# Kernel optimization log

Hardware: AMD Instinct MI355X
Metric: run time of the kernel (lower is better)

The kernel has to match this reference:

```python
import jax, jax.numpy as jnp
import numpy as np

HID, NH, QLR, KVLR, QK, VH, RH = 7168, 128, 1536, 512, 128, 128, 64
EPS = 1.1920929e-07  # torch.finfo(float32).eps, RMSNorm eps=None default
ROPE_BASE = 10000.0


def _rmsnorm(x, w):
    return x * jax.lax.rsqrt(jnp.mean(x * x, axis=-1, keepdims=True) + EPS) * w


def _rope_tables(seq_len, dim):
    inv_freq = 1.0 / (ROPE_BASE ** (np.arange(0, dim, 2, dtype=np.float32) / dim))
    t = np.arange(seq_len, dtype=np.float32)
    freqs = np.outer(t, inv_freq)          # [S, dim/2]
    emb = np.concatenate([freqs, freqs], -1)  # [S, dim]
    return jnp.asarray(np.cos(emb)), jnp.asarray(np.sin(emb))


def _apply_rope(x, cos, sin):
    # x: [B, H, S, D]; rotate-half convention matching the torch module
    d = x.shape[-1]
    x1, x2 = x[..., : d // 2], x[..., d // 2 :]
    rotated = jnp.concatenate([-x2, x1], axis=-1)
    return x * cos + rotated * sin


def setup_inputs() -> dict:
    key = jax.random.key(0)
    ks = jax.random.split(key, 9)
    def w(k, out_dim, in_dim):
        return jax.random.normal(k, (out_dim, in_dim), jnp.float32) / np.sqrt(in_dim)
    return {
        "hidden_states": jax.random.normal(ks[0], (1, 1024, HID), jnp.float32),
        "w_q_down": w(ks[1], QLR, HID),
        "q_norm_w": jnp.ones((QLR,), jnp.float32),
        "w_q_up": w(ks[2], NH * (QK + RH), QLR),
        "w_kv_down": w(ks[3], KVLR + RH, HID),
        "kv_norm_w": jnp.ones((KVLR,), jnp.float32),
        "w_kv_up": w(ks[4], NH * (QK + VH), KVLR),
        "w_out": w(ks[5], HID, NH * VH),
    }


def reference(hidden_states, w_q_down, q_norm_w, w_q_up, w_kv_down, kv_norm_w, w_kv_up, w_out):
    B, S, _ = hidden_states.shape
    cos, sin = _rope_tables(S, RH)

    # Q path: down -> RMSNorm -> up, split into non-rope / rope parts
    c_q = jnp.einsum("bsh,qh->bsq", hidden_states, w_q_down)            # [B,S,QLR]
    q_cr = jnp.einsum("bsq,oq->bso", _rmsnorm(c_q, q_norm_w), w_q_up)   # [B,S,NH*(QK+RH)]
    q_cr = q_cr.reshape(B, S, NH, QK + RH).transpose(0, 2, 1, 3)        # [B,NH,S,QK+RH]
    q_c, q_r = q_cr[..., :QK], q_cr[..., QK:]

    # KV path: shared latent + MQA rope key
    ckv_kr = jnp.einsum("bsh,oh->bso", hidden_states, w_kv_down)        # [B,S,KVLR+RH]
    c_kv, k_r = ckv_kr[..., :KVLR], ckv_kr[..., KVLR:]
    k_r = k_r[:, None, :, :]                                            # [B,1,S,RH]
    kv = jnp.einsum("bsq,oq->bso", _rmsnorm(c_kv, kv_norm_w), w_kv_up)  # [B,S,NH*(QK+VH)]
    kv = kv.reshape(B, S, NH, QK + VH).transpose(0, 2, 1, 3)            # [B,NH,S,QK+VH]
    k_c, v = kv[..., :QK], kv[..., QK:]

    q_r = _apply_rope(q_r, cos, sin)
    k_r = _apply_rope(k_r, cos, sin)

    q = jnp.concatenate([q_c, q_r], axis=-1)                            # [B,NH,S,QK+RH]
    k = jnp.concatenate([k_c, jnp.broadcast_to(k_r, (B, NH, S, RH))], axis=-1)

    scale = 1.0 / np.sqrt(QK + RH)
    scores = jnp.einsum("bhqd,bhkd->bhqk", q, k) * scale
    attn = jax.nn.softmax(scores, axis=-1)
    o = jnp.einsum("bhqk,bhkd->bhqd", attn, v)                          # [B,NH,S,VH]
    o = o.transpose(0, 2, 1, 3).reshape(B, S, NH * VH)
    return jnp.einsum("bso,ho->bsh", o, w_out)
```

## Files before the change

kernel.cpp:

```cpp
#include <hip/hip_runtime.h>
#include <hip/hip_bf16.h>
#include <math.h>

#define HIDN 7168
#define NHEAD 128
#define QLRANK 1536
#define KVLRANK 512
#define QKD 128
#define VHD 128
#define RHD 64
#define SEQ 1024
#define RMS_EPS 1.1920929e-07f

typedef unsigned short u16;
typedef __attribute__((ext_vector_type(8))) short bf16x8;
typedef __attribute__((ext_vector_type(4))) float f32x4;
typedef __attribute__((ext_vector_type(8))) unsigned short u16x8;

__device__ __forceinline__ u16 f2bf(float f) {
    unsigned int u = __float_as_uint(f);
    unsigned int r = (u + 0x7FFFu + ((u >> 16) & 1u)) >> 16;
    return (u16)r;
}
__device__ __forceinline__ float bf2f(u16 v) {
    return __uint_as_float(((unsigned int)v) << 16);
}

__device__ __forceinline__ void gld_lds16(const u16* g, u16* l) {
    __builtin_amdgcn_global_load_lds(
        (const __attribute__((address_space(1))) unsigned int*)g,
        (__attribute__((address_space(3))) unsigned int*)l,
        16, 0, 0);
}

__global__ __launch_bounds__(256) void f32_to_bf16(const float* __restrict__ in,
                                                   u16* __restrict__ out, long n) {
    long i = ((long)blockIdx.x * blockDim.x + threadIdx.x) * 8;
    long stride = (long)gridDim.x * blockDim.x * 8;
    for (; i < n; i += stride) {
        float4 a = *(const float4*)(in + i);
        float4 b = *(const float4*)(in + i + 4);
        u16x8 o;
        o[0] = f2bf(a.x); o[1] = f2bf(a.y); o[2] = f2bf(a.z); o[3] = f2bf(a.w);
        o[4] = f2bf(b.x); o[5] = f2bf(b.y); o[6] = f2bf(b.z); o[7] = f2bf(b.w);
        *(u16x8*)(out + i) = o;
    }
}

template <int OUT_BF16>
__global__ __launch_bounds__(256) void gemm_bt(const u16* __restrict__ A,
                                               const u16* __restrict__ B,
                                               void* __restrict__ Cv,
                                               int M, int N, int Kslice, long ldk) {
    __shared__ u16 As[2 * 128 * 64];
    __shared__ u16 Bs[2 * 128 * 64];
    const int tid = threadIdx.x;
    const int lane = tid & 63;
    const int w = tid >> 6;
    const int wr = w >> 1, wc = w & 1;
    const int l15 = lane & 15, lg = lane >> 4;
    const int n0 = blockIdx.x * 128;
    const int m0 = blockIdx.y * 128;
    const long kbase = (long)blockIdx.z * Kslice;

    const u16* asrc[4];
    const u16* bsrc[4];
    int aoff[4];
#pragma unroll
    for (int i = 0; i < 4; ++i) {
        int r = (w * 4 + i) * 8 + (lane >> 3);
        int gc = (lane & 7) ^ (r & 7);
        asrc[i] = A + (long)(m0 + r) * ldk + kbase + gc * 8;
        int br = n0 + r; if (br >= N) br = N - 1;
        bsrc[i] = B + (long)br * ldk + kbase + gc * 8;
        aoff[i] = (w * 4 + i) * 512;
    }

    f32x4 acc[4][4];
    const f32x4 z = {0.f, 0.f, 0.f, 0.f};
#pragma unroll
    for (int i = 0; i < 4; ++i)
#pragma unroll
        for (int j = 0; j < 4; ++j) acc[i][j] = z;

    auto stage = [&](int bufi, int kofs) {
#pragma unroll
        for (int i = 0; i < 4; ++i) {
            gld_lds16(asrc[i] + kofs, As + bufi * 8192 + aoff[i]);
            gld_lds16(bsrc[i] + kofs, Bs + bufi * 8192 + aoff[i]);
        }
    };

    const int nsteps = Kslice >> 6;
    stage(0, 0);
    asm volatile("s_waitcnt vmcnt(0)" ::: "memory");
    __builtin_amdgcn_s_barrier();

    int cur = 0;
    for (int t = 0; t < nsteps; ++t) {
        if (t + 1 < nsteps) stage(cur ^ 1, (t + 1) * 64);
        const u16* Ab = As + cur * 8192;
        const u16* Bb = Bs + cur * 8192;
#pragma unroll
        for (int kk = 0; kk < 2; ++kk) {
            bf16x8 a[4], b[4];
#pragma unroll
            for (int i = 0; i < 4; ++i) {
                int row = wr * 64 + i * 16 + l15;
                a[i] = *(const bf16x8*)&Ab[row * 64 + ((kk * 4 + lg) ^ (row & 7)) * 8];
            }
#pragma unroll
            for (int j = 0; j < 4; ++j) {
                int row = wc * 64 + j * 16 + l15;
                b[j] = *(const bf16x8*)&Bb[row * 64 + ((kk * 4 + lg) ^ (row & 7)) * 8];
            }
#pragma unroll
            for (int i = 0; i < 4; ++i)
#pragma unroll
                for (int j = 0; j < 4; ++j)
                    acc[i][j] = __builtin_amdgcn_mfma_f32_16x16x32_bf16(a[i], b[j], acc[i][j], 0, 0, 0);
        }
        asm volatile("s_waitcnt vmcnt(0)" ::: "memory");
        __builtin_amdgcn_s_barrier();
        cur ^= 1;
    }

#pragma unroll
    for (int i = 0; i < 4; ++i)
#pragma unroll
        for (int j = 0; j < 4; ++j)
#pragma unroll
            for (int r = 0; r < 4; ++r) {
                int m = m0 + wr * 64 + i * 16 + lg * 4 + r;
                int n = n0 + wc * 64 + j * 16 + l15;
                if (n < N) {
                    if (OUT_BF16)
                        ((u16*)Cv)[(long)m * N + n] = f2bf(acc[i][j][r]);
                    else
                        ((float*)Cv)[(long)blockIdx.z * M * N + (long)m * N + n] = acc[i][j][r];
                }
            }
}

__global__ __launch_bounds__(256) void reduce_parts(const float* __restrict__ parts,
                                                    float* __restrict__ out,
                                                    int nparts, long mn) {
    long i = ((long)blockIdx.x * 256 + threadIdx.x) * 4;
    long stride = (long)gridDim.x * 256 * 4;
    for (; i < mn; i += stride) {
        float4 s = *(const float4*)(parts + i);
        for (int p = 1; p < nparts; ++p) {
            float4 v = *(const float4*)(parts + (long)p * mn + i);
            s.x += v.x; s.y += v.y; s.z += v.z; s.w += v.w;
        }
        *(float4*)(out + i) = s;
    }
}

__global__ __launch_bounds__(256) void rmsnorm_kernel(const float* __restrict__ x,
                                                      const float* __restrict__ w,
                                                      u16* __restrict__ y,
                                                      int stride, int norm_len) {
    const int row = blockIdx.x;
    const float* xr = x + (long)row * stride;
    float ss = 0.f;
    for (int i = threadIdx.x; i < norm_len; i += 256) {
        float v = xr[i];
        ss += v * v;
    }
#pragma unroll
    for (int off = 32; off > 0; off >>= 1) ss += __shfl_down(ss, off);
    __shared__ float partial[4];
    if ((threadIdx.x & 63) == 0) partial[threadIdx.x >> 6] = ss;
    __syncthreads();
    float tot = partial[0] + partial[1] + partial[2] + partial[3];
    float rs = 1.0f / sqrtf(tot / (float)norm_len + RMS_EPS);
    u16* yr = y + (long)row * norm_len;
    for (int i = threadIdx.x; i < norm_len; i += 256) yr[i] = f2bf(xr[i] * rs * w[i]);
}

__global__ void rope_tables(float* __restrict__ cos_t, float* __restrict__ sin_t) {
    int s = blockIdx.x;
    int i = threadIdx.x;
    float invf = powf(10000.0f, -((float)(2 * i) / 64.0f));
    float ang = (float)s * invf;
    cos_t[s * 32 + i] = cosf(ang);
    sin_t[s * 32 + i] = sinf(ang);
}

__global__ void rope_q(u16* __restrict__ q_cr, const float* __restrict__ cos_t,
                       const float* __restrict__ sin_t) {
    int s = blockIdx.x;
    int h = blockIdx.y * 2 + (threadIdx.x >> 5);
    int i = threadIdx.x & 31;
    u16* base = q_cr + (s * (NHEAD * 192) + h * 192 + QKD);
    float x1 = bf2f(base[i]);
    float x2 = bf2f(base[i + 32]);
    float c = cos_t[s * 32 + i], sn = sin_t[s * 32 + i];
    base[i]      = f2bf(x1 * c - x2 * sn);
    base[i + 32] = f2bf(x2 * c + x1 * sn);
}

__global__ void rope_k(const float* __restrict__ ckv_kr, const float* __restrict__ cos_t,
                       const float* __restrict__ sin_t, u16* __restrict__ kr) {
    int s = blockIdx.x;
    int i = threadIdx.x;
    if (i < 32) {
        const float* base = ckv_kr + (s * 576 + 512);
        float x1 = base[i], x2 = base[i + 32];
        float c = cos_t[s * 32 + i], sn = sin_t[s * 32 + i];
        kr[s * 64 + i]      = f2bf(x1 * c - x2 * sn);
        kr[s * 64 + i + 32] = f2bf(x2 * c + x1 * sn);
    }
}

__global__ __launch_bounds__(256) void build_vt(const u16* __restrict__ kv,
                                                u16* __restrict__ vT) {
    __shared__ u16 vtile[64][136];
    const int h = blockIdx.x, sb = blockIdx.y, s0 = sb * 64;
    const int tid = threadIdx.x;
#pragma unroll
    for (int it = 0; it < 4; ++it) {
        int c = it * 256 + tid;
        int row = c >> 4;
        int off8 = (c & 15) * 8;
        *(u16x8*)&vtile[row][off8] =
            *(const u16x8*)&kv[(s0 + row) * 32768 + h * 256 + 128 + off8];
    }
    __syncthreads();
    const int sl = tid & 63;
    const int dvb = tid >> 6;
#pragma unroll
    for (int it = 0; it < 32; ++it) {
        int dv = dvb + it * 4;
        vT[(h * 128 + dv) * 1024 + s0 + sl] = vtile[sl][dv];
    }
}

__global__ __launch_bounds__(512) void mla_attn(const u16* __restrict__ q_cr,
                                                const u16* __restrict__ kv,
                                                const u16* __restrict__ kr,
                                                const u16* __restrict__ vT,
                                                u16* __restrict__ o_g) {
    __shared__ u16 ks[64][200];
    __shared__ u16 vts[128][72];
    __shared__ u16 p_lds[8][16][72];
    const int qb = blockIdx.x, h = blockIdx.y;
    const int s0q = qb * 128;
    const int tid = threadIdx.x, lane = tid & 63, w = tid >> 6;
    const int l15 = lane & 15, lg = lane >> 4;
    const float scale = 0.07216878364870323f;

    bf16x8 qreg[6];
    {
        const int qrow = s0q + w * 16 + l15;
#pragma unroll
        for (int kk = 0; kk < 6; ++kk)
            qreg[kk] = *(const bf16x8*)&q_cr[qrow * (NHEAD * 192) + h * 192 + kk * 32 + lg * 8];
    }

    const int krow0 = tid >> 4,           koff0 = (tid & 15) * 8;
    const int krow1 = (512 + tid) >> 4,   koff1 = ((512 + tid) & 15) * 8;
    const int rrow  = tid >> 3,           roff  = (tid & 7) * 8;
    const int vdv0  = tid >> 3,           voff0 = (tid & 7) * 8;
    const int vdv1  = (512 + tid) >> 3,   voff1 = ((512 + tid) & 7) * 8;
    const u16* kvp = kv + h * 256;
    const u16* vtp = vT + (long)(h * 128) * 1024;

    u16x8 kreg0, kreg1, krreg, vreg0, vreg1;
    auto load_tile = [&](int s0k) {
        kreg0 = *(const u16x8*)&kvp[(long)(s0k + krow0) * 32768 + koff0];
        kreg1 = *(const u16x8*)&kvp[(long)(s0k + krow1) * 32768 + koff1];
        krreg = *(const u16x8*)&kr[(s0k + rrow) * 64 + roff];
        vreg0 = *(const u16x8*)&vtp[(long)vdv0 * 1024 + s0k + voff0];
        vreg1 = *(const u16x8*)&vtp[(long)vdv1 * 1024 + s0k + voff1];
    };

    f32x4 o_acc[8];
    const f32x4 z = {0.f, 0.f, 0.f, 0.f};
#pragma unroll
    for (int d = 0; d < 8; ++d) o_acc[d] = z;
    float m_r[4], l_r[4];
#pragma unroll
    for (int r = 0; r < 4; ++r) { m_r[r] = -1e30f; l_r[r] = 0.f; }

    load_tile(0);

    for (int kt = 0; kt < 16; ++kt) {
        __syncthreads();
        *(u16x8*)&ks[krow0][koff0]      = kreg0;
        *(u16x8*)&ks[krow1][koff1]      = kreg1;
        *(u16x8*)&ks[rrow][128 + roff]  = krreg;
        *(u16x8*)&vts[vdv0][voff0]      = vreg0;
        *(u16x8*)&vts[vdv1][voff1]      = vreg1;
        __syncthreads();
        if (kt + 1 < 16) load_tile((kt + 1) * 64);

        f32x4 sf[4];
#pragma unroll
        for (int j = 0; j < 4; ++j) sf[j] = z;
#pragma unroll
        for (int kk = 0; kk < 6; ++kk) {
            bf16x8 a = qreg[kk];
#pragma unroll
            for (int j = 0; j < 4; ++j) {
                bf16x8 b = *(const bf16x8*)&ks[j * 16 + l15][kk * 32 + lg * 8];
                sf[j] = __builtin_amdgcn_mfma_f32_16x16x32_bf16(a, b, sf[j], 0, 0, 0);
            }
        }

        float p[4][4];
        float alpha[4];
#pragma unroll
        for (int r = 0; r < 4; ++r) {
            float mx = fmaxf(fmaxf(sf[0][r], sf[1][r]), fmaxf(sf[2][r], sf[3][r]));
#pragma unroll
            for (int off = 1; off < 16; off <<= 1) mx = fmaxf(mx, __shfl_xor(mx, off));
            mx *= scale;
            float mnew = fmaxf(m_r[r], mx);
            alpha[r] = __expf(m_r[r] - mnew);
            float rs = 0.f;
#pragma unroll
            for (int j = 0; j < 4; ++j) {
                float pv = __expf(sf[j][r] * scale - mnew);
                p[j][r] = pv;
                rs += pv;
            }
#pragma unroll
            for (int off = 1; off < 16; off <<= 1) rs += __shfl_xor(rs, off);
            l_r[r] = l_r[r] * alpha[r] + rs;
            m_r[r] = mnew;
        }
#pragma unroll
        for (int d = 0; d < 8; ++d)
#pragma unroll
            for (int r = 0; r < 4; ++r) o_acc[d][r] *= alpha[r];

#pragma unroll
        for (int j = 0; j < 4; ++j)
#pragma unroll
            for (int r = 0; r < 4; ++r)
                p_lds[w][lg * 4 + r][j * 16 + l15] = f2bf(p[j][r]);

#pragma unroll
        for (int kk2 = 0; kk2 < 2; ++kk2) {
            bf16x8 a = *(const bf16x8*)&p_lds[w][l15][kk2 * 32 + lg * 8];
#pragma unroll
            for (int d = 0; d < 8; ++d) {
                bf16x8 b = *(const bf16x8*)&vts[d * 16 + l15][kk2 * 32 + lg * 8];
                o_acc[d] = __builtin_amdgcn_mfma_f32_16x16x32_bf16(a, b, o_acc[d], 0, 0, 0);
            }
        }
    }

#pragma unroll
    for (int d = 0; d < 8; ++d)
#pragma unroll
        for (int r = 0; r < 4; ++r) {
            int srow = s0q + w * 16 + lg * 4 + r;
            float v = o_acc[d][r] / l_r[r];
            o_g[srow * 16384 + h * 128 + d * 16 + l15] = f2bf(v);
        }
}

extern "C" void kernel_launch(void* const* d_in, const int* in_sizes, int n_in,
                              void* d_out, int out_size, void* d_ws, size_t ws_size,
                              hipStream_t stream) {
    const float* hs        = (const float*)d_in[0];
    const float* w_q_down  = (const float*)d_in[1];
    const float* q_norm_w  = (const float*)d_in[2];
    const float* w_q_up    = (const float*)d_in[3];
    const float* w_kv_down = (const float*)d_in[4];
    const float* kv_norm_w = (const float*)d_in[5];
    const float* w_kv_up   = (const float*)d_in[6];
    const float* w_out     = (const float*)d_in[7];
    float* out = (float*)d_out;
    char* ws = (char*)d_ws;

    const size_t SZ_HS   = (size_t)SEQ * HIDN * 2;
    const size_t SZ_KV   = (size_t)SEQ * 32768 * 2;
    const size_t SZ_QCR  = (size_t)SEQ * (NHEAD * 192) * 2;
    const size_t SZ_VT   = (size_t)NHEAD * 128 * 1024 * 2;
    const size_t SZ_WB   = (size_t)24576 * 1536 * 2;
    const size_t SZ_CQ   = (size_t)SEQ * QLRANK * 4;
    const size_t SZ_CQN  = (size_t)SEQ * QLRANK * 2;
    const size_t SZ_CKV  = (size_t)SEQ * 576 * 4;
    const size_t SZ_CKVN = (size_t)SEQ * KVLRANK * 2;
    const size_t SZ_KR   = (size_t)SEQ * 64 * 2;
    const size_t SZ_OG   = (size_t)SEQ * 16384 * 2;
    const size_t SZ_TAB  = (size_t)SEQ * 32 * 4;

    size_t off = 0;
    u16* hs_bf  = (u16*)(ws + off); off += SZ_HS;
    u16* kvb    = (u16*)(ws + off); off += SZ_KV;
    u16* q_cr   = (u16*)(ws + off); off += SZ_QCR;
    u16* vT     = (u16*)(ws + off); off += SZ_VT;
    u16* W_BUF  = (u16*)(ws + off); off += SZ_WB;
    float* parts = (float*)((char*)W_BUF + 33554432);
    u16* wout_bf = (u16*)ws;
    float* c_q    = (float*)(ws + off); off += SZ_CQ;
    u16* cq_n     = (u16*)(ws + off); off += SZ_CQN;
    float* ckv_kr = (float*)(ws + off); off += SZ_CKV;
    u16* ckv_n    = (u16*)(ws + off); off += SZ_CKVN;
    u16* kr       = (u16*)(ws + off); off += SZ_KR;
    u16* o_g      = (u16*)(ws + off); off += SZ_OG;
    float* cos_t  = (float*)(ws + off); off += SZ_TAB;
    float* sin_t  = (float*)(ws + off); off += SZ_TAB;
    const size_t SZ_POP = (size_t)2 * SEQ * HIDN * 4;
    float* parts_op = (float*)(ws + off);
    const bool splitOP = (off + SZ_POP) <= ws_size;
    (void)in_sizes; (void)n_in; (void)out_size;

    rope_tables<<<dim3(SEQ), dim3(32), 0, stream>>>(cos_t, sin_t);
    f32_to_bf16<<<2048, 256, 0, stream>>>(hs, hs_bf, (long)SEQ * HIDN);

    f32_to_bf16<<<2048, 256, 0, stream>>>(w_q_down, W_BUF, (long)QLRANK * HIDN);
    gemm_bt<0><<<dim3(QLRANK / 128, SEQ / 128, 4), 256, 0, stream>>>(hs_bf, W_BUF, parts, SEQ, QLRANK, HIDN / 4, HIDN);
    reduce_parts<<<1024, 256, 0, stream>>>(parts, c_q, 4, (long)SEQ * QLRANK);
    rmsnorm_kernel<<<SEQ, 256, 0, stream>>>(c_q, q_norm_w, cq_n, QLRANK, QLRANK);

    f32_to_bf16<<<2048, 256, 0, stream>>>(w_q_up, W_BUF, (long)24576 * QLRANK);
    gemm_bt<1><<<dim3(24576 / 128, SEQ / 128), 256, 0, stream>>>(cq_n, W_BUF, q_cr, SEQ, 24576, QLRANK, QLRANK);

    f32_to_bf16<<<2048, 256, 0, stream>>>(w_kv_down, W_BUF, (long)576 * HIDN);
    gemm_bt<0><<<dim3(5, SEQ / 128, 8), 256, 0, stream>>>(hs_bf, W_BUF, parts, SEQ, 576, HIDN / 8, HIDN);
    reduce_parts<<<1024, 256, 0, stream>>>(parts, ckv_kr, 8, (long)SEQ * 576);
    rmsnorm_kernel<<<SEQ, 256, 0, stream>>>(ckv_kr, kv_norm_w, ckv_n, 576, KVLRANK);
    rope_k<<<SEQ, 64, 0, stream>>>(ckv_kr, cos_t, sin_t, kr);

    f32_to_bf16<<<2048, 256, 0, stream>>>(w_kv_up, W_BUF, (long)32768 * KVLRANK);
    gemm_bt<1><<<dim3(32768 / 128, SEQ / 128), 256, 0, stream>>>(ckv_n, W_BUF, kvb, SEQ, 32768, KVLRANK, KVLRANK);

    rope_q<<<dim3(SEQ, NHEAD / 2), 64, 0, stream>>>(q_cr, cos_t, sin_t);
    build_vt<<<dim3(NHEAD, SEQ / 64), 256, 0, stream>>>(kvb, vT);

    mla_attn<<<dim3(SEQ / 128, NHEAD), 512, 0, stream>>>(q_cr, kvb, kr, vT, o_g);

    f32_to_bf16<<<2048, 256, 0, stream>>>(w_out, wout_bf, (long)HIDN * 16384);
    if (splitOP) {
        gemm_bt<0><<<dim3(HIDN / 128, SEQ / 128, 2), 256, 0, stream>>>(o_g, wout_bf, parts_op, SEQ, HIDN, 16384 / 2, 16384);
        reduce_parts<<<1024, 256, 0, stream>>>(parts_op, out, 2, (long)SEQ * HIDN);
    } else {
        gemm_bt<0><<<dim3(HIDN / 128, SEQ / 128), 256, 0, stream>>>(o_g, wout_bf, out, SEQ, HIDN, 16384, 16384);
    }
}
```

Measured before the change: 1.022 ms.

## Single-buffer GEMM LDS, allow 4-way split-K for output projection

The GEMM drops its double-buffered LDS staging for a single buffer with load, sync, compute, sync per K-step. This halves shared memory per block, which may let more blocks share a CU, but global loads no longer overlap with MFMA work. The output projection can now split K four ways when the workspace allows, adding parallelism at the cost of more partial-sum traffic and a larger reduction. The w_out conversion launch uses more blocks.

```diff
diff --git a/kernel.cpp b/kernel.cpp
--- a/kernel.cpp
+++ b/kernel.cpp
@@ -52,8 +52,8 @@
                                                const u16* __restrict__ B,
                                                void* __restrict__ Cv,
                                                int M, int N, int Kslice, long ldk) {
-    __shared__ u16 As[2 * 128 * 64];
-    __shared__ u16 Bs[2 * 128 * 64];
+    __shared__ u16 As[128 * 64];
+    __shared__ u16 Bs[128 * 64];
     const int tid = threadIdx.x;
     const int lane = tid & 63;
     const int w = tid >> 6;
@@ -83,36 +83,25 @@
 #pragma unroll
         for (int j = 0; j < 4; ++j) acc[i][j] = z;
 
-    auto stage = [&](int bufi, int kofs) {
+    for (int k0 = 0; k0 < Kslice; k0 += 64) {
 #pragma unroll
         for (int i = 0; i < 4; ++i) {
-            gld_lds16(asrc[i] + kofs, As + bufi * 8192 + aoff[i]);
-            gld_lds16(bsrc[i] + kofs, Bs + bufi * 8192 + aoff[i]);
-        }
-    };
-
-    const int nsteps = Kslice >> 6;
-    stage(0, 0);
-    asm volatile("s_waitcnt vmcnt(0)" ::: "memory");
-    __builtin_amdgcn_s_barrier();
-
-    int cur = 0;
-    for (int t = 0; t < nsteps; ++t) {
-        if (t + 1 < nsteps) stage(cur ^ 1, (t + 1) * 64);
-        const u16* Ab = As + cur * 8192;
-        const u16* Bb = Bs + cur * 8192;
+            gld_lds16(asrc[i] + k0, As + aoff[i]);
+            gld_lds16(bsrc[i] + k0, Bs + aoff[i]);
+        }
+        __syncthreads();
 #pragma unroll
         for (int kk = 0; kk < 2; ++kk) {
             bf16x8 a[4], b[4];
 #pragma unroll
             for (int i = 0; i < 4; ++i) {
                 int row = wr * 64 + i * 16 + l15;
-                a[i] = *(const bf16x8*)&Ab[row * 64 + ((kk * 4 + lg) ^ (row & 7)) * 8];
+                a[i] = *(const bf16x8*)&As[row * 64 + ((kk * 4 + lg) ^ (row & 7)) * 8];
             }
 #pragma unroll
             for (int j = 0; j < 4; ++j) {
                 int row = wc * 64 + j * 16 + l15;
-                b[j] = *(const bf16x8*)&Bb[row * 64 + ((kk * 4 + lg) ^ (row & 7)) * 8];
+                b[j] = *(const bf16x8*)&Bs[row * 64 + ((kk * 4 + lg) ^ (row & 7)) * 8];
             }
 #pragma unroll
             for (int i = 0; i < 4; ++i)
@@ -120,9 +109,7 @@
                 for (int j = 0; j < 4; ++j)
                     acc[i][j] = __builtin_amdgcn_mfma_f32_16x16x32_bf16(a[i], b[j], acc[i][j], 0, 0, 0);
         }
-        asm volatile("s_waitcnt vmcnt(0)" ::: "memory");
-        __builtin_amdgcn_s_barrier();
-        cur ^= 1;
+        __syncthreads();
     }
 
 #pragma unroll
@@ -406,9 +393,11 @@
     u16* o_g      = (u16*)(ws + off); off += SZ_OG;
     float* cos_t  = (float*)(ws + off); off += SZ_TAB;
     float* sin_t  = (float*)(ws + off); off += SZ_TAB;
-    const size_t SZ_POP = (size_t)2 * SEQ * HIDN * 4;
     float* parts_op = (float*)(ws + off);
-    const bool splitOP = (off + SZ_POP) <= ws_size;
+    const size_t szp1 = (size_t)SEQ * HIDN * 4;
+    int nsplit = 1;
+    if (off + 4 * szp1 <= ws_size) nsplit = 4;
+    else if (off + 2 * szp1 <= ws_size) nsplit = 2;
     (void)in_sizes; (void)n_in; (void)out_size;
 
     rope_tables<<<dim3(SEQ), dim3(32), 0, stream>>>(cos_t, sin_t);
@@ -436,10 +425,10 @@
 
     mla_attn<<<dim3(SEQ / 128, NHEAD), 512, 0, stream>>>(q_cr, kvb, kr, vT, o_g);
 
-    f32_to_bf16<<<2048, 256, 0, stream>>>(w_out, wout_bf, (long)HIDN * 16384);
-    if (splitOP) {
-        gemm_bt<0><<<dim3(HIDN / 128, SEQ / 128, 2), 256, 0, stream>>>(o_g, wout_bf, parts_op, SEQ, HIDN, 16384 / 2, 16384);
-        reduce_parts<<<1024, 256, 0, stream>>>(parts_op, out, 2, (long)SEQ * HIDN);
+    f32_to_bf16<<<4096, 256, 0, stream>>>(w_out, wout_bf, (long)HIDN * 16384);
+    if (nsplit > 1) {
+        gemm_bt<0><<<dim3(HIDN / 128, SEQ / 128, nsplit), 256, 0, stream>>>(o_g, wout_bf, parts_op, SEQ, HIDN, 16384 / nsplit, 16384);
+        reduce_parts<<<1024, 256, 0, stream>>>(parts_op, out, nsplit, (long)SEQ * HIDN);
     } else {
         gemm_bt<0><<<dim3(HIDN / 128, SEQ / 128), 256, 0, stream>>>(o_g, wout_bf, out, SEQ, HIDN, 16384, 16384);
     }
```

After: 1.061 ms. 1.04x slower.
